# Kernel optimization log

Measured on AMD Instinct MI355X. Metric: run time of the kernel, lower is better.

Reference implementation:

```python
import jax, jax.numpy as jnp
import numpy as np

N = 262144       # nodes (4096 graphs * graph_deg 64)
E = 4194304      # edges
D = 64           # node_dim
DEPTH = 3
GRAPH_DEG = 64


def gcn_conv(x, W, b, src, dst, w):
    """PyG GCNConv with self-loops + symmetric norm; masked edges have w=0."""
    h = x @ W                                             # [N, D]
    deg = jax.ops.segment_sum(w, dst, num_segments=N) + 1.0  # +1 self-loop
    dinv = jax.lax.rsqrt(deg)                             # deg >= 1
    norm = dinv[src] * w * dinv[dst]                      # [E]
    agg = jax.ops.segment_sum(h[src] * norm[:, None], dst, num_segments=N)
    agg = agg + h * (dinv * dinv)[:, None]                # self-loop term
    return agg + b


def setup_inputs() -> dict:
    key = jax.random.key(0)
    ks = jax.random.split(key, 24)

    def xavier(k, fan_in, fan_out):
        lim = np.sqrt(6.0 / (fan_in + fan_out))
        return jax.random.uniform(k, (fan_in, fan_out), jnp.float32, -lim, lim)

    inp = {
        "x": jax.random.normal(ks[0], (N, 1), jnp.float32),
        "edge_index": jax.random.randint(ks[1], (2, E), 0, N, jnp.int64),
        "edge_types": jax.random.randint(ks[2], (E,), 0, 5, jnp.int64),
        "node_W": xavier(ks[3], 1, D), "node_b": jnp.zeros((D,), jnp.float32),
        "out1_W": xavier(ks[4], D, D), "out1_b": jnp.zeros((D,), jnp.float32),
        "out2_W": xavier(ks[5], D, 1), "out2_b": jnp.zeros((1,), jnp.float32),
    }
    names = ["W1", "W2", "W3", "W4", "W2b", "W3b", "W4b"]
    for i, n in enumerate(names):
        inp[n] = xavier(ks[6 + i], D, D)
        inp["b" + n[1:]] = jnp.zeros((D,), jnp.float32)
    return inp


def reference(x, edge_index, edge_types,
              node_W, node_b,
              W1, b1, W2, b2, W3, b3, W4, b4,
              W2b, b2b, W3b, b3b, W4b, b4b,
              out1_W, out1_b, out2_W, out2_b):
    src, dst = edge_index[0], edge_index[1]
    w1 = (edge_types == 1).astype(jnp.float32)
    w2 = (edge_types == 2).astype(jnp.float32)
    w3 = (edge_types == 3).astype(jnp.float32)
    w4 = (edge_types == 4).astype(jnp.float32)

    h = x @ node_W + node_b                               # [N, D]
    for _ in range(DEPTH):
        h_new = (gcn_conv(h, W1, b1, src, dst, w1)
                 + gcn_conv(h, W2, b2, src, dst, w2)
                 + gcn_conv(h, W3, b3, src, dst, w3)
                 + gcn_conv(h, W4, b4, src, dst, w4)
                 + gcn_conv(h, W2b, b2b, dst, src, w2)    # reversed edges
                 + gcn_conv(h, W3b, b3b, dst, src, w3)
                 + gcn_conv(h, W4b, b4b, dst, src, w4))
        h = jax.nn.relu(h_new)

    g = h.reshape(-1, GRAPH_DEG, D)                       # [B, deg, D]
    g = jnp.max(g, axis=1)                                # [B, D]
    g = jax.nn.relu(g @ out1_W + out1_b)
    return g @ out2_W + out2_b                            # [B, 1]
```

## Files before the change

kernel.cpp:

```cpp
#include <hip/hip_runtime.h>
#include <stdint.h>

typedef unsigned int u32;
typedef unsigned short u16;
typedef __attribute__((ext_vector_type(8))) short bf16x8;
typedef __attribute__((ext_vector_type(4))) float f32x4;

#define BCAP 16384u

struct Ptr7 { const float* p[7]; };

__device__ __forceinline__ int rfl(int v) { return __builtin_amdgcn_readfirstlane(v); }
__device__ __forceinline__ u16 f2bf(float f) {
    u32 u = __float_as_uint(f);
    u32 r = (u + 0x7FFFu + ((u >> 16) & 1u)) >> 16;
    return (u16)r;
}
__device__ __forceinline__ float bf2f(u16 h) { return __uint_as_float((u32)h << 16); }


__global__ void k_init_cur(u32* __restrict__ g) {
    int i = blockIdx.x * 256 + threadIdx.x;
    if (i < 512) g[i] = (u32)i << 14;
}

__global__ __launch_bounds__(256)
void k_passA(const int* __restrict__ ei, const int* __restrict__ ty, int E,
             u32* __restrict__ gcursor, u32* __restrict__ tmpItems) {
    __shared__ u32 hist[512], gb[512], cur[512];
    int tid = threadIdx.x;
    int e0 = blockIdx.x * 8192;
    hist[tid] = 0; hist[tid + 256] = 0;
    __syncthreads();
#pragma unroll
    for (int i = 0; i < 32; i++) {
        int e = e0 + i * 256 + tid;
        if (e < E) {
            int s = ei[e], d = ei[E + e], t = ty[e];
            if (t >= 1) atomicAdd(&hist[(u32)d >> 9], 1u);
            if (t >= 2) atomicAdd(&hist[(u32)s >> 9], 1u);
        }
    }
    __syncthreads();
    u32 h0 = hist[tid], h1 = hist[tid + 256];
    gb[tid] = h0 ? atomicAdd(&gcursor[tid], h0) : 0u;
    gb[tid + 256] = h1 ? atomicAdd(&gcursor[tid + 256], h1) : 0u;
    cur[tid] = 0; cur[tid + 256] = 0;
    __syncthreads();
#pragma unroll
    for (int i = 0; i < 32; i++) {
        int e = e0 + i * 256 + tid;
        if (e < E) {
            int s = ei[e], d = ei[E + e], t = ty[e];
            if (t >= 1) {
                u32 b = (u32)d >> 9;
                u32 slot = atomicAdd(&cur[b], 1u);
                u32 pos = gb[b] + slot;
                if (pos < ((b + 1u) << 14))
                    tmpItems[pos] = (u32)s | ((u32)(t - 1) << 18) | (((u32)d & 511u) << 21);
            }
            if (t >= 2) {
                u32 b = (u32)s >> 9;
                u32 slot = atomicAdd(&cur[b], 1u);
                u32 pos = gb[b] + slot;
                if (pos < ((b + 1u) << 14))
                    tmpItems[pos] = (u32)d | ((u32)(t + 2) << 18) | (((u32)s & 511u) << 21);
            }
        }
    }
}

__global__ __launch_bounds__(256)
void k_passB(const u32* __restrict__ tmpItems, const u32* __restrict__ bucketEnd,
             float* __restrict__ dinv, u16* __restrict__ dinv16,
             u32* __restrict__ kcnt, int N) {
    __shared__ u32 c[512 * 8];
    int b = blockIdx.x, tid = threadIdx.x;
    for (int i = tid; i < 4096; i += 256) c[i] = 0;
    __syncthreads();
    u32 beg = (u32)b << 14;
    u32 end = bucketEnd[b];
    u32 cap = beg + BCAP;
    if (end > cap) end = cap;
    for (u32 i = beg + tid; i < end; i += 256) {
        u32 it = tmpItems[i];
        atomicAdd(&c[(it >> 21) * 8 + ((it >> 18) & 7)], 1u);
    }
    __syncthreads();
    int nodeBase = b << 9;
    for (int i = tid; i < 4096; i += 256) kcnt[(size_t)b * 4096 + i] = c[i];
    for (int l = tid; l < 512; l += 256) {
        int n = nodeBase + l;
#pragma unroll
        for (int k = 0; k < 7; k++) {
            float v = rsqrtf(1.0f + (float)c[l * 8 + k]);
            dinv[k * N + n] = v;
            dinv16[k * N + n] = f2bf(v);
        }
    }
}

__global__ __launch_bounds__(256)
void k_scan1(const u32* __restrict__ kcnt, u32* __restrict__ kofs, u32* __restrict__ bsums) {
    __shared__ u32 lds[256];
    int t = threadIdx.x;
    size_t base = (size_t)blockIdx.x * 8192 + (size_t)t * 32;
    u32 v[32];
    u32 s = 0;
    const uint4* src = (const uint4*)(kcnt + base);
#pragma unroll
    for (int q = 0; q < 8; q++) {
        uint4 c4 = src[q];
        v[q * 4 + 0] = s; s += c4.x;
        v[q * 4 + 1] = s; s += c4.y;
        v[q * 4 + 2] = s; s += c4.z;
        v[q * 4 + 3] = s; s += c4.w;
    }
    lds[t] = s; __syncthreads();
    for (int off = 1; off < 256; off <<= 1) {
        u32 x2 = (t >= off) ? lds[t - off] : 0u;
        __syncthreads();
        lds[t] += x2;
        __syncthreads();
    }
    u32 texcl = lds[t] - s;
    uint4* dst = (uint4*)(kofs + base);
#pragma unroll
    for (int q = 0; q < 8; q++) {
        uint4 o;
        o.x = v[q * 4 + 0] + texcl; o.y = v[q * 4 + 1] + texcl;
        o.z = v[q * 4 + 2] + texcl; o.w = v[q * 4 + 3] + texcl;
        dst[q] = o;
    }
    if (t == 255) bsums[blockIdx.x] = lds[255];
}

__global__ void k_scan2(const u32* __restrict__ bsums, u32* __restrict__ bexcl, int nb) {
    __shared__ u32 lds[256];
    int t = threadIdx.x;
    u32 v = (t < nb) ? bsums[t] : 0u;
    lds[t] = v; __syncthreads();
    for (int off = 1; off < 256; off <<= 1) {
        u32 x2 = (t >= off) ? lds[t - off] : 0u;
        __syncthreads();
        lds[t] += x2;
        __syncthreads();
    }
    if (t < nb) bexcl[t] = lds[t] - v;
}

__global__ __launch_bounds__(256)
void k_scan3(u32* __restrict__ kofs, const u32* __restrict__ bexcl,
             const u32* __restrict__ bsums, u32 M) {
    int t = threadIdx.x;
    size_t base = (size_t)blockIdx.x * 8192 + (size_t)t * 32;
    u32 add = bexcl[blockIdx.x];
    uint4* p4 = (uint4*)(kofs + base);
#pragma unroll
    for (int q = 0; q < 8; q++) {
        uint4 o = p4[q];
        o.x += add; o.y += add; o.z += add; o.w += add;
        p4[q] = o;
    }
    if (blockIdx.x == 255 && t == 255) kofs[M] = add + bsums[255];
}

__global__ __launch_bounds__(256)
void k_passC(const u32* __restrict__ tmpItems, const u32* __restrict__ bucketEnd,
             const u32* __restrict__ kofs, u32* __restrict__ entries) {
    __shared__ u32 cur[4096];
    int b = blockIdx.x, tid = threadIdx.x;
    for (int i = tid; i < 4096; i += 256) cur[i] = kofs[(size_t)b * 4096 + i];
    __syncthreads();
    u32 beg = (u32)b << 14;
    u32 end = bucketEnd[b];
    u32 cap = beg + BCAP;
    if (end > cap) end = cap;
    for (u32 i = beg + tid; i < end; i += 256) {
        u32 it = tmpItems[i];
        u32 p = atomicAdd(&cur[(it >> 21) * 8 + ((it >> 18) & 7)], 1u);
        entries[p] = it & 0x1FFFFFu;
    }
}

__global__ __launch_bounds__(256)
void k_coef_pq(const u32* __restrict__ entries, const u32* __restrict__ kofs,
               const u16* __restrict__ dinv16, const float* __restrict__ dinv,
               const float* __restrict__ x, u16* __restrict__ coef16,
               float* __restrict__ P, float* __restrict__ Q, int N) {
    int i = blockIdx.x * 256 + threadIdx.x;
    u32 beg = kofs[i], end = kofs[i + 1];
    int k = i & 7, n = i >> 3;
    float sP = 0.f, sQ = 0.f;
    for (u32 p = beg; p < end; ++p) {
        u32 src = entries[p] & 0x3FFFFu;
        u16 cb = dinv16[(size_t)k * N + src];
        coef16[p] = cb;
        float cf = bf2f(cb);
        sP += cf * x[src];
        sQ += cf;
    }
    if (k < 7) {
        float dk = dinv[k * N + n];
        float xn = x[n];
        P[i] = dk * (sP + dk * xn);
        Q[i] = dk * (sQ + dk);
    }
}

__global__ void k_bsum(Ptr7 b, float* __restrict__ bsum) {
    int d = threadIdx.x;
    float s = 0.f;
#pragma unroll
    for (int k = 0; k < 7; k++) s += b.p[k][d];
    bsum[d] = s;
}

__global__ void k_uv(const float* __restrict__ nW, const float* __restrict__ nb,
                     Ptr7 W, float* __restrict__ U, float* __restrict__ V) {
    int k = blockIdx.x, d = threadIdx.x;
    const float* Wk = W.p[k];
    float u = 0.f, v = 0.f;
#pragma unroll 8
    for (int j = 0; j < 64; j++) {
        float w = Wk[j * 64 + d];
        u += nW[j] * w;
        v += nb[j] * w;
    }
    U[k * 64 + d] = u;
    V[k * 64 + d] = v;
}

__global__ void k_packW(Ptr7 W, u16* __restrict__ Wp) {
    int k = blockIdx.x;
    int tid = threadIdx.x;
    int ks = tid >> 8, ct = (tid >> 6) & 3, l = tid & 63;
    const float* Wk = W.p[k];
    u16* dst = Wp + (((size_t)(k * 2 + ks) * 4 + ct) * 512 + l * 8);
    int row0 = ks * 32 + (l >> 4) * 8;
    int col = ct * 16 + (l & 15);
#pragma unroll
    for (int i = 0; i < 8; i++) dst[i] = f2bf(Wk[(row0 + i) * 64 + col]);
}

__global__ __launch_bounds__(256)
void k_h1(const float* __restrict__ P, const float* __restrict__ Q,
          const float* __restrict__ U, const float* __restrict__ V,
          const float* __restrict__ bsum, u16* __restrict__ h1) {
    int i = blockIdx.x * 256 + threadIdx.x;
    int n = rfl(i >> 6);
    int d = i & 63;
    float acc = bsum[d];
#pragma unroll
    for (int k = 0; k < 7; k++)
        acc += P[n * 8 + k] * U[k * 64 + d] + Q[n * 8 + k] * V[k * 64 + d];
    h1[((size_t)n << 6) + d] = f2bf(fmaxf(acc, 0.f));
}

#define GACC(PK, CB, HV)                                             \
    {                                                                \
        float cf_ = __uint_as_float((u32)(CB) << 16);                \
        switch ((PK) >> 18) {                                        \
            case 0: a0 = fmaf(cf_, (HV), a0); break;                 \
            case 1: a1 = fmaf(cf_, (HV), a1); break;                 \
            case 2: a2 = fmaf(cf_, (HV), a2); break;                 \
            case 3: a3 = fmaf(cf_, (HV), a3); break;                 \
            case 4: a4 = fmaf(cf_, (HV), a4); break;                 \
            case 5: a5 = fmaf(cf_, (HV), a5); break;                 \
            default: a6 = fmaf(cf_, (HV), a6); break;                \
        }                                                            \
    }

__global__ __launch_bounds__(256)
void k_gather(const u16* __restrict__ h, const u32* __restrict__ entries,
              const u16* __restrict__ coef16, const u32* __restrict__ kofs,
              const float* __restrict__ dinv, u16* __restrict__ m, int N, int c0) {
    int lane = threadIdx.x & 63;
    int nl = blockIdx.x * 4 + (threadIdx.x >> 6);
    int n = c0 + nl;
    u32 beg = (u32)rfl((int)kofs[(size_t)n << 3]);
    u32 end = (u32)rfl((int)kofs[((size_t)n << 3) + 7]);
    float hv = bf2f(h[((size_t)n << 6) + lane]);
    float d0 = dinv[n],         d1 = dinv[N + n],     d2 = dinv[2 * N + n];
    float d3 = dinv[3 * N + n], d4 = dinv[4 * N + n], d5 = dinv[5 * N + n];
    float d6 = dinv[6 * N + n];
    float a0 = d0 * hv, a1 = d1 * hv, a2 = d2 * hv, a3 = d3 * hv;
    float a4 = d4 * hv, a5 = d5 * hv, a6 = d6 * hv;

    u32 base = beg;
    u32 e = 0, cfw = 0;
    if (base + (u32)lane < end) {
        e = entries[base + lane];
        cfw = (u32)coef16[base + lane];
    }
    while (base < end) {
        u32 rem = end - base;
        int cnt = (rem < 64u) ? (int)rem : 64;
        u32 nb2 = base + 64;
        u32 en = 0, cfn = 0;
        if (nb2 + (u32)lane < end) {
            en = entries[nb2 + lane];
            cfn = (u32)coef16[nb2 + lane];
        }
        int j = 0;
        for (; j + 8 <= cnt; j += 8) {
            u32 pk0 = (u32)__builtin_amdgcn_readlane((int)e, j + 0);
            u32 pk1 = (u32)__builtin_amdgcn_readlane((int)e, j + 1);
            u32 pk2 = (u32)__builtin_amdgcn_readlane((int)e, j + 2);
            u32 pk3 = (u32)__builtin_amdgcn_readlane((int)e, j + 3);
            u32 pk4 = (u32)__builtin_amdgcn_readlane((int)e, j + 4);
            u32 pk5 = (u32)__builtin_amdgcn_readlane((int)e, j + 5);
            u32 pk6 = (u32)__builtin_amdgcn_readlane((int)e, j + 6);
            u32 pk7 = (u32)__builtin_amdgcn_readlane((int)e, j + 7);
            u32 cb0 = (u32)__builtin_amdgcn_readlane((int)cfw, j + 0);
            u32 cb1 = (u32)__builtin_amdgcn_readlane((int)cfw, j + 1);
            u32 cb2 = (u32)__builtin_amdgcn_readlane((int)cfw, j + 2);
            u32 cb3 = (u32)__builtin_amdgcn_readlane((int)cfw, j + 3);
            u32 cb4 = (u32)__builtin_amdgcn_readlane((int)cfw, j + 4);
            u32 cb5 = (u32)__builtin_amdgcn_readlane((int)cfw, j + 5);
            u32 cb6 = (u32)__builtin_amdgcn_readlane((int)cfw, j + 6);
            u32 cb7 = (u32)__builtin_amdgcn_readlane((int)cfw, j + 7);
            float h0 = bf2f(h[((size_t)(pk0 & 0x3FFFFu) << 6) + lane]);
            float h1v = bf2f(h[((size_t)(pk1 & 0x3FFFFu) << 6) + lane]);
            float h2v = bf2f(h[((size_t)(pk2 & 0x3FFFFu) << 6) + lane]);
            float h3v = bf2f(h[((size_t)(pk3 & 0x3FFFFu) << 6) + lane]);
            float h4v = bf2f(h[((size_t)(pk4 & 0x3FFFFu) << 6) + lane]);
            float h5v = bf2f(h[((size_t)(pk5 & 0x3FFFFu) << 6) + lane]);
            float h6v = bf2f(h[((size_t)(pk6 & 0x3FFFFu) << 6) + lane]);
            float h7v = bf2f(h[((size_t)(pk7 & 0x3FFFFu) << 6) + lane]);
            GACC(pk0, cb0, h0)
            GACC(pk1, cb1, h1v)
            GACC(pk2, cb2, h2v)
            GACC(pk3, cb3, h3v)
            GACC(pk4, cb4, h4v)
            GACC(pk5, cb5, h5v)
            GACC(pk6, cb6, h6v)
            GACC(pk7, cb7, h7v)
        }
        for (; j + 4 <= cnt; j += 4) {
            u32 pk0 = (u32)__builtin_amdgcn_readlane((int)e, j + 0);
            u32 pk1 = (u32)__builtin_amdgcn_readlane((int)e, j + 1);
            u32 pk2 = (u32)__builtin_amdgcn_readlane((int)e, j + 2);
            u32 pk3 = (u32)__builtin_amdgcn_readlane((int)e, j + 3);
            u32 cb0 = (u32)__builtin_amdgcn_readlane((int)cfw, j + 0);
            u32 cb1 = (u32)__builtin_amdgcn_readlane((int)cfw, j + 1);
            u32 cb2 = (u32)__builtin_amdgcn_readlane((int)cfw, j + 2);
            u32 cb3 = (u32)__builtin_amdgcn_readlane((int)cfw, j + 3);
            float h0 = bf2f(h[((size_t)(pk0 & 0x3FFFFu) << 6) + lane]);
            float h1v = bf2f(h[((size_t)(pk1 & 0x3FFFFu) << 6) + lane]);
            float h2v = bf2f(h[((size_t)(pk2 & 0x3FFFFu) << 6) + lane]);
            float h3v = bf2f(h[((size_t)(pk3 & 0x3FFFFu) << 6) + lane]);
            GACC(pk0, cb0, h0)
            GACC(pk1, cb1, h1v)
            GACC(pk2, cb2, h2v)
            GACC(pk3, cb3, h3v)
        }
        for (; j < cnt; ++j) {
            u32 pk = (u32)__builtin_amdgcn_readlane((int)e, j);
            u32 cb = (u32)__builtin_amdgcn_readlane((int)cfw, j);
            float hval = bf2f(h[((size_t)(pk & 0x3FFFFu) << 6) + lane]);
            GACC(pk, cb, hval)
        }
        e = en; cfw = cfn; base = nb2;
    }

    u16* mp = m + (size_t)nl * 448 + lane;
    __builtin_nontemporal_store(f2bf(d0 * a0), mp);
    __builtin_nontemporal_store(f2bf(d1 * a1), mp + 64);
    __builtin_nontemporal_store(f2bf(d2 * a2), mp + 128);
    __builtin_nontemporal_store(f2bf(d3 * a3), mp + 192);
    __builtin_nontemporal_store(f2bf(d4 * a4), mp + 256);
    __builtin_nontemporal_store(f2bf(d5 * a5), mp + 320);
    __builtin_nontemporal_store(f2bf(d6 * a6), mp + 384);
}

__global__ __launch_bounds__(256)
void k_gemm(const u16* __restrict__ m, const u16* __restrict__ Wp,
            const float* __restrict__ bsum, u16* __restrict__ hout, int c0) {
    int tid = threadIdx.x;
    int w = tid >> 6, l = tid & 63;
    int nb = blockIdx.x << 6;
    const u16* arow = m + (size_t)(nb + (w << 4) + (l & 15)) * 448 + ((l >> 4) << 3);
    const u16* bp = Wp + (size_t)l * 8;
    f32x4 acc0 = {0,0,0,0}, acc1 = {0,0,0,0}, acc2 = {0,0,0,0}, acc3 = {0,0,0,0};
#pragma unroll
    for (int kk = 0; kk < 14; kk++) {
        bf16x8 a  = __builtin_nontemporal_load((const bf16x8*)(arow + kk * 32));
        bf16x8 b0 = *(const bf16x8*)(bp + (size_t)(kk * 4 + 0) * 512);
        bf16x8 b1 = *(const bf16x8*)(bp + (size_t)(kk * 4 + 1) * 512);
        bf16x8 b2 = *(const bf16x8*)(bp + (size_t)(kk * 4 + 2) * 512);
        bf16x8 b3 = *(const bf16x8*)(bp + (size_t)(kk * 4 + 3) * 512);
        acc0 = __builtin_amdgcn_mfma_f32_16x16x32_bf16(a, b0, acc0, 0, 0, 0);
        acc1 = __builtin_amdgcn_mfma_f32_16x16x32_bf16(a, b1, acc1, 0, 0, 0);
        acc2 = __builtin_amdgcn_mfma_f32_16x16x32_bf16(a, b2, acc2, 0, 0, 0);
        acc3 = __builtin_amdgcn_mfma_f32_16x16x32_bf16(a, b3, acc3, 0, 0, 0);
    }
    int rl = (l >> 4) << 2, cl = l & 15;
    int rowg = c0 + nb + (w << 4) + rl;
    f32x4 accs[4] = {acc0, acc1, acc2, acc3};
#pragma unroll
    for (int ct = 0; ct < 4; ct++) {
        int col = ct * 16 + cl;
        float bv = bsum[col];
#pragma unroll
        for (int reg = 0; reg < 4; reg++) {
            float vv = fmaxf(accs[ct][reg] + bv, 0.f);
            hout[(size_t)(rowg + reg) * 64 + col] = f2bf(vv);
        }
    }
}

__global__ __launch_bounds__(256)
void k_head(const u16* __restrict__ h, const float* __restrict__ w1,
            const float* __restrict__ b1, const float* __restrict__ w2,
            const float* __restrict__ b2, float* __restrict__ out) {
    __shared__ float gmax[4][64];
    __shared__ float gl[64];
    __shared__ float t1p[4][64];
    int b = blockIdx.x;
    int tid = threadIdx.x;
    int d = tid & 63, rg = tid >> 6;
    const u16* hb = h + (size_t)b * 64 * 64;
    float pm = -1e30f;
#pragma unroll
    for (int i = 0; i < 16; i++) pm = fmaxf(pm, bf2f(hb[(rg * 16 + i) * 64 + d]));
    gmax[rg][d] = pm; __syncthreads();
    if (rg == 0) gl[d] = fmaxf(fmaxf(gmax[0][d], gmax[1][d]), fmaxf(gmax[2][d], gmax[3][d]));
    __syncthreads();
    float s = 0.f;
#pragma unroll
    for (int i = 0; i < 16; i++) { int dd = rg * 16 + i; s += gl[dd] * w1[dd * 64 + d]; }
    t1p[rg][d] = s; __syncthreads();
    if (rg == 0) {
        float t1 = fmaxf(t1p[0][d] + t1p[1][d] + t1p[2][d] + t1p[3][d] + b1[d], 0.f);
        float v = t1 * w2[d];
        for (int off = 32; off; off >>= 1) v += __shfl_down(v, off, 64);
        if (d == 0) out[b] = v + b2[0];
    }
}

extern "C" void kernel_launch(void* const* d_in, const int* in_sizes, int n_in,
                              void* d_out, int out_size, void* d_ws, size_t ws_size,
                              hipStream_t stream) {
    const float* x     = (const float*)d_in[0];
    const int*   ei    = (const int*)d_in[1];
    const int*   ty    = (const int*)d_in[2];
    const float* nodeW = (const float*)d_in[3];
    const float* nodeb = (const float*)d_in[4];
    const float* out1W = (const float*)d_in[5];
    const float* out1b = (const float*)d_in[6];
    const float* out2W = (const float*)d_in[7];
    const float* out2b = (const float*)d_in[8];

    Ptr7 W, B;
    W.p[0] = (const float*)d_in[9];  B.p[0] = (const float*)d_in[10];
    W.p[1] = (const float*)d_in[11]; B.p[1] = (const float*)d_in[12];
    W.p[2] = (const float*)d_in[13]; B.p[2] = (const float*)d_in[14];
    W.p[3] = (const float*)d_in[15]; B.p[3] = (const float*)d_in[16];
    W.p[4] = (const float*)d_in[17]; B.p[4] = (const float*)d_in[18];
    W.p[5] = (const float*)d_in[19]; B.p[5] = (const float*)d_in[20];
    W.p[6] = (const float*)d_in[21]; B.p[6] = (const float*)d_in[22];

    const int N = in_sizes[0];
    const int E = in_sizes[2];

    char* p = (char*)d_ws;
    auto carve = [&](size_t bytes) { void* r = (void*)p; p += (bytes + 255) & ~(size_t)255; return r; };
    u16*   hA       = (u16*)carve((size_t)N * 64 * 2);
    u16*   hB       = (u16*)carve((size_t)N * 64 * 2);
    u32*   entries  = (u32*)carve((size_t)2 * E * 4);
    u16*   coef16   = (u16*)carve((size_t)2 * E * 2);
    float* dinv     = (float*)carve((size_t)7 * N * 4);
    u16*   dinv16   = (u16*)carve((size_t)7 * N * 2);
    u32*   kcnt     = (u32*)carve((size_t)8 * N * 4);
    u32*   kofs     = (u32*)carve(((size_t)8 * N + 1) * 4);
    float* P        = (float*)carve((size_t)N * 8 * 4);
    float* Q        = (float*)carve((size_t)N * 8 * 4);
    float* U        = (float*)carve(7 * 64 * 4);
    float* V        = (float*)carve(7 * 64 * 4);
    float* bsum     = (float*)carve(256);
    u16*   Wp       = (u16*)carve((size_t)7 * 2 * 4 * 512 * 2);
    u32*   gcursor  = (u32*)carve(512 * 4);
    u32*   bsums    = (u32*)carve(1024);
    u32*   bexcl    = (u32*)carve(1024);
    size_t used = (size_t)(p - (char*)d_ws);
    size_t avail = (ws_size > used) ? (ws_size - used) : 0;
    u32*   tmpItems = (u32*)p;
    u16*   m        = (u16*)p;
    size_t chunkNodes = (avail / (448 * 2)) & ~(size_t)63;
    if (chunkNodes < 64) chunkNodes = 64;
    if (chunkNodes > 65536) chunkNodes = 65536;
    if (chunkNodes > (size_t)N) chunkNodes = (size_t)N;
    (void)n_in; (void)out_size;

    k_init_cur<<<2, 256, 0, stream>>>(gcursor);
    k_passA<<<(E + 8191) / 8192, 256, 0, stream>>>(ei, ty, E, gcursor, tmpItems);
    k_passB<<<512, 256, 0, stream>>>(tmpItems, gcursor, dinv, dinv16, kcnt, N);
    k_scan1<<<256, 256, 0, stream>>>(kcnt, kofs, bsums);
    k_scan2<<<1, 256, 0, stream>>>(bsums, bexcl, 256);
    k_scan3<<<256, 256, 0, stream>>>(kofs, bexcl, bsums, (u32)8 * N);
    k_passC<<<512, 256, 0, stream>>>(tmpItems, gcursor, kofs, entries);
    k_coef_pq<<<(8 * N) / 256, 256, 0, stream>>>(entries, kofs, dinv16, dinv, x,
                                                 coef16, P, Q, N);

    k_bsum<<<1, 64, 0, stream>>>(B, bsum);
    k_uv<<<7, 64, 0, stream>>>(nodeW, nodeb, W, U, V);
    k_packW<<<7, 512, 0, stream>>>(W, Wp);

    k_h1<<<(N * 64) / 256, 256, 0, stream>>>(P, Q, U, V, bsum, hA);

    u16* hcur = hA;
    u16* hnext = hB;
    for (int depth = 0; depth < 2; depth++) {
        for (int c0 = 0; c0 < N; c0 += (int)chunkNodes) {
            int cn = (int)(((size_t)(N - c0) < chunkNodes) ? (size_t)(N - c0) : chunkNodes);
            k_gather<<<cn / 4, 256, 0, stream>>>(hcur, entries, coef16, kofs, dinv, m, N, c0);
            k_gemm<<<cn / 64, 256, 0, stream>>>(m, Wp, bsum, hnext, c0);
        }
        u16* t = hcur; hcur = hnext; hnext = t;
    }

    k_head<<<N / 64, 256, 0, stream>>>(hcur, out1W, out1b, out2W, out2b, (float*)d_out);
}
```

Measured before the change: 949.5 us.

## Register-cache edges in passA, pre-shift gather offsets, nontemporal entry loads, bigger chunks

passA now loads each edge once into registers and reuses it for both the histogram and scatter phases, with half the edges per block and twice the blocks. Entries now store the source pre-shifted into a byte offset (src<<7) with the type in the top bits, so the gather computes the h address with one mask and add instead of a shift chain. Entry and coefficient loads in the gather use nontemporal hints to avoid polluting cache needed for h rows. The chunk-size cap is raised so fewer gather/GEMM chunk launches are needed, at the cost of a larger m buffer.

Measured after the change: 943.5 us. Within noise of the previous version (-0.6%).

```diff
diff --git a/kernel.cpp b/kernel.cpp
--- a/kernel.cpp
+++ b/kernel.cpp
@@ -29,17 +29,20 @@
              u32* __restrict__ gcursor, u32* __restrict__ tmpItems) {
     __shared__ u32 hist[512], gb[512], cur[512];
     int tid = threadIdx.x;
-    int e0 = blockIdx.x * 8192;
+    int e0 = blockIdx.x * 4096;
+    int s[16], d[16], t[16];
+#pragma unroll
+    for (int i = 0; i < 16; i++) {
+        int e = e0 + i * 256 + tid;
+        if (e < E) { s[i] = ei[e]; d[i] = ei[E + e]; t[i] = ty[e]; }
+        else t[i] = 0;
+    }
     hist[tid] = 0; hist[tid + 256] = 0;
     __syncthreads();
 #pragma unroll
-    for (int i = 0; i < 32; i++) {
-        int e = e0 + i * 256 + tid;
-        if (e < E) {
-            int s = ei[e], d = ei[E + e], t = ty[e];
-            if (t >= 1) atomicAdd(&hist[(u32)d >> 9], 1u);
-            if (t >= 2) atomicAdd(&hist[(u32)s >> 9], 1u);
-        }
+    for (int i = 0; i < 16; i++) {
+        if (t[i] >= 1) atomicAdd(&hist[(u32)d[i] >> 9], 1u);
+        if (t[i] >= 2) atomicAdd(&hist[(u32)s[i] >> 9], 1u);
     }
     __syncthreads();
     u32 h0 = hist[tid], h1 = hist[tid + 256];
@@ -48,24 +51,20 @@
     cur[tid] = 0; cur[tid + 256] = 0;
     __syncthreads();
 #pragma unroll
-    for (int i = 0; i < 32; i++) {
-        int e = e0 + i * 256 + tid;
-        if (e < E) {
-            int s = ei[e], d = ei[E + e], t = ty[e];
-            if (t >= 1) {
-                u32 b = (u32)d >> 9;
-                u32 slot = atomicAdd(&cur[b], 1u);
-                u32 pos = gb[b] + slot;
-                if (pos < ((b + 1u) << 14))
-                    tmpItems[pos] = (u32)s | ((u32)(t - 1) << 18) | (((u32)d & 511u) << 21);
-            }
-            if (t >= 2) {
-                u32 b = (u32)s >> 9;
-                u32 slot = atomicAdd(&cur[b], 1u);
-                u32 pos = gb[b] + slot;
-                if (pos < ((b + 1u) << 14))
-                    tmpItems[pos] = (u32)d | ((u32)(t + 2) << 18) | (((u32)s & 511u) << 21);
-            }
+    for (int i = 0; i < 16; i++) {
+        if (t[i] >= 1) {
+            u32 b = (u32)d[i] >> 9;
+            u32 slot = atomicAdd(&cur[b], 1u);
+            u32 pos = gb[b] + slot;
+            if (pos < ((b + 1u) << 14))
+                tmpItems[pos] = (u32)s[i] | ((u32)(t[i] - 1) << 18) | (((u32)d[i] & 511u) << 21);
+        }
+        if (t[i] >= 2) {
+            u32 b = (u32)s[i] >> 9;
+            u32 slot = atomicAdd(&cur[b], 1u);
+            u32 pos = gb[b] + slot;
+            if (pos < ((b + 1u) << 14))
+                tmpItems[pos] = (u32)d[i] | ((u32)(t[i] + 2) << 18) | (((u32)s[i] & 511u) << 21);
         }
     }
 }
@@ -178,8 +177,10 @@
     if (end > cap) end = cap;
     for (u32 i = beg + tid; i < end; i += 256) {
         u32 it = tmpItems[i];
-        u32 p = atomicAdd(&cur[(it >> 21) * 8 + ((it >> 18) & 7)], 1u);
-        entries[p] = it & 0x1FFFFFu;
+        u32 k = (it >> 18) & 7u;
+        u32 src = it & 0x3FFFFu;
+        u32 p = atomicAdd(&cur[(it >> 21) * 8 + k], 1u);
+        entries[p] = (k << 28) | (src << 7);
     }
 }
 
@@ -193,7 +194,7 @@
     int k = i & 7, n = i >> 3;
     float sP = 0.f, sQ = 0.f;
     for (u32 p = beg; p < end; ++p) {
-        u32 src = entries[p] & 0x3FFFFu;
+        u32 src = (entries[p] >> 7) & 0x3FFFFu;
         u16 cb = dinv16[(size_t)k * N + src];
         coef16[p] = cb;
         float cf = bf2f(cb);
@@ -260,7 +261,7 @@
 #define GACC(PK, CB, HV)                                             \
     {                                                                \
         float cf_ = __uint_as_float((u32)(CB) << 16);                \
-        switch ((PK) >> 18) {                                        \
+        switch ((PK) >> 28) {                                        \
             case 0: a0 = fmaf(cf_, (HV), a0); break;                 \
             case 1: a1 = fmaf(cf_, (HV), a1); break;                 \
             case 2: a2 = fmaf(cf_, (HV), a2); break;                 \
@@ -270,6 +271,7 @@
             default: a6 = fmaf(cf_, (HV), a6); break;                \
         }                                                            \
     }
+#define HLOAD(PK) bf2f(*(const u16*)(hb + ((PK) & 0x01FFFFFFu)))
 
 __global__ __launch_bounds__(256)
 void k_gather(const u16* __restrict__ h, const u32* __restrict__ entries,
@@ -278,6 +280,7 @@
     int lane = threadIdx.x & 63;
     int nl = blockIdx.x * 4 + (threadIdx.x >> 6);
     int n = c0 + nl;
+    const char* hb = (const char*)h + 2 * lane;
     u32 beg = (u32)rfl((int)kofs[(size_t)n << 3]);
     u32 end = (u32)rfl((int)kofs[((size_t)n << 3) + 7]);
     float hv = bf2f(h[((size_t)n << 6) + lane]);
@@ -290,8 +293,8 @@
     u32 base = beg;
     u32 e = 0, cfw = 0;
     if (base + (u32)lane < end) {
-        e = entries[base + lane];
-        cfw = (u32)coef16[base + lane];
+        e = __builtin_nontemporal_load(&entries[base + lane]);
+        cfw = (u32)__builtin_nontemporal_load(&coef16[base + lane]);
     }
     while (base < end) {
         u32 rem = end - base;
@@ -299,8 +302,8 @@
         u32 nb2 = base + 64;
         u32 en = 0, cfn = 0;
         if (nb2 + (u32)lane < end) {
-            en = entries[nb2 + lane];
-            cfn = (u32)coef16[nb2 + lane];
+            en = __builtin_nontemporal_load(&entries[nb2 + lane]);
+            cfn = (u32)__builtin_nontemporal_load(&coef16[nb2 + lane]);
         }
         int j = 0;
         for (; j + 8 <= cnt; j += 8) {
@@ -320,14 +323,14 @@
             u32 cb5 = (u32)__builtin_amdgcn_readlane((int)cfw, j + 5);
             u32 cb6 = (u32)__builtin_amdgcn_readlane((int)cfw, j + 6);
             u32 cb7 = (u32)__builtin_amdgcn_readlane((int)cfw, j + 7);
-            float h0 = bf2f(h[((size_t)(pk0 & 0x3FFFFu) << 6) + lane]);
-            float h1v = bf2f(h[((size_t)(pk1 & 0x3FFFFu) << 6) + lane]);
-            float h2v = bf2f(h[((size_t)(pk2 & 0x3FFFFu) << 6) + lane]);
-            float h3v = bf2f(h[((size_t)(pk3 & 0x3FFFFu) << 6) + lane]);
-            float h4v = bf2f(h[((size_t)(pk4 & 0x3FFFFu) << 6) + lane]);
-            float h5v = bf2f(h[((size_t)(pk5 & 0x3FFFFu) << 6) + lane]);
-            float h6v = bf2f(h[((size_t)(pk6 & 0x3FFFFu) << 6) + lane]);
-            float h7v = bf2f(h[((size_t)(pk7 & 0x3FFFFu) << 6) + lane]);
+            float h0 = HLOAD(pk0);
+            float h1v = HLOAD(pk1);
+            float h2v = HLOAD(pk2);
+            float h3v = HLOAD(pk3);
+            float h4v = HLOAD(pk4);
+            float h5v = HLOAD(pk5);
+            float h6v = HLOAD(pk6);
+            float h7v = HLOAD(pk7);
             GACC(pk0, cb0, h0)
             GACC(pk1, cb1, h1v)
             GACC(pk2, cb2, h2v)
@@ -346,10 +349,10 @@
             u32 cb1 = (u32)__builtin_amdgcn_readlane((int)cfw, j + 1);
             u32 cb2 = (u32)__builtin_amdgcn_readlane((int)cfw, j + 2);
             u32 cb3 = (u32)__builtin_amdgcn_readlane((int)cfw, j + 3);
-            float h0 = bf2f(h[((size_t)(pk0 & 0x3FFFFu) << 6) + lane]);
-            float h1v = bf2f(h[((size_t)(pk1 & 0x3FFFFu) << 6) + lane]);
-            float h2v = bf2f(h[((size_t)(pk2 & 0x3FFFFu) << 6) + lane]);
-            float h3v = bf2f(h[((size_t)(pk3 & 0x3FFFFu) << 6) + lane]);
+            float h0 = HLOAD(pk0);
+            float h1v = HLOAD(pk1);
+            float h2v = HLOAD(pk2);
+            float h3v = HLOAD(pk3);
             GACC(pk0, cb0, h0)
             GACC(pk1, cb1, h1v)
             GACC(pk2, cb2, h2v)
@@ -358,7 +361,7 @@
         for (; j < cnt; ++j) {
             u32 pk = (u32)__builtin_amdgcn_readlane((int)e, j);
             u32 cb = (u32)__builtin_amdgcn_readlane((int)cfw, j);
-            float hval = bf2f(h[((size_t)(pk & 0x3FFFFu) << 6) + lane]);
+            float hval = HLOAD(pk);
             GACC(pk, cb, hval)
         }
         e = en; cfw = cfn; base = nb2;
@@ -468,8 +471,8 @@
     auto carve = [&](size_t bytes) { void* r = (void*)p; p += (bytes + 255) & ~(size_t)255; return r; };
     u16*   hA       = (u16*)carve((size_t)N * 64 * 2);
     u16*   hB       = (u16*)carve((size_t)N * 64 * 2);
-    u32*   entries  = (u32*)carve((size_t)2 * E * 4);
-    u16*   coef16   = (u16*)carve((size_t)2 * E * 2);
+    u32*   entries  = (u32*)carve((size_t)2 * E * 4 + 256);
+    u16*   coef16   = (u16*)carve((size_t)2 * E * 2 + 128);
     float* dinv     = (float*)carve((size_t)7 * N * 4);
     u16*   dinv16   = (u16*)carve((size_t)7 * N * 2);
     u32*   kcnt     = (u32*)carve((size_t)8 * N * 4);
@@ -489,12 +492,12 @@
     u16*   m        = (u16*)p;
     size_t chunkNodes = (avail / (448 * 2)) & ~(size_t)63;
     if (chunkNodes < 64) chunkNodes = 64;
-    if (chunkNodes > 65536) chunkNodes = 65536;
+    if (chunkNodes > 131072) chunkNodes = 131072;
     if (chunkNodes > (size_t)N) chunkNodes = (size_t)N;
     (void)n_in; (void)out_size;
 
     k_init_cur<<<2, 256, 0, stream>>>(gcursor);
-    k_passA<<<(E + 8191) / 8192, 256, 0, stream>>>(ei, ty, E, gcursor, tmpItems);
+    k_passA<<<(E + 4095) / 4096, 256, 0, stream>>>(ei, ty, E, gcursor, tmpItems);
     k_passB<<<512, 256, 0, stream>>>(tmpItems, gcursor, dinv, dinv16, kcnt, N);
     k_scan1<<<256, 256, 0, stream>>>(kcnt, kofs, bsums);
     k_scan2<<<1, 256, 0, stream>>>(bsums, bexcl, 256);
```
